# Optimization experiments

Measured on AMD Instinct MI355X. Metric: run time of the kernel, lower is better.

The kernel has to match this reference:

```python
import jax, jax.numpy as jnp
import numpy as np

BS, N_LINKS, MAX_LEN = 8192, 512, 32
D_LINK, D_PATH, D_READ, N_OUT = 32, 128, 256, 3
BN_EPS = 1e-5


def setup_inputs() -> dict:
    key = jax.random.key(0)
    ks = jax.random.split(key, 16)
    capa = jax.random.uniform(ks[0], (BS, N_LINKS), jnp.float32, 0.5, 1.0) * 100.0
    avail = jax.random.uniform(ks[1], (BS, N_LINKS), jnp.float32) * capa
    loss = jax.random.uniform(ks[2], (BS, N_LINKS), jnp.float32) * 0.05
    demand = jax.random.uniform(ks[3], (BS,), jnp.float32) * 10.0
    path = jax.random.randint(ks[4], (BS, MAX_LEN), 0, N_LINKS)
    hop_num = jax.random.randint(ks[5], (BS,), 1, MAX_LEN + 1)
    s = 0.1
    inp = {
        "demand": demand,
        "link_avail_capacity": avail,
        "link_capacity": capa,
        "link_loss": loss,
        "path": path,
        "hop_num": hop_num,
        # GRU params (PyTorch layout: [3H, D] gates ordered r,z,n)
        "gru_w_ih": jax.random.normal(ks[6], (3 * D_PATH, D_LINK), jnp.float32) * s,
        "gru_w_hh": jax.random.normal(ks[7], (3 * D_PATH, D_PATH), jnp.float32) * s,
        "gru_b_ih": jax.random.normal(ks[8], (3 * D_PATH,), jnp.float32) * s,
        "gru_b_hh": jax.random.normal(ks[9], (3 * D_PATH,), jnp.float32) * s,
        "bn_gamma": jnp.ones((D_PATH,), jnp.float32),
        "bn_beta": jnp.zeros((D_PATH,), jnp.float32),
        # stacked readout heads [N_OUT, ...]
        "rW1": jax.random.normal(ks[10], (N_OUT, D_PATH, D_READ), jnp.float32) * s,
        "rb1": jnp.zeros((N_OUT, D_READ), jnp.float32),
        "rW2": jax.random.normal(ks[11], (N_OUT, D_READ, D_READ), jnp.float32) * s,
        "rb2": jnp.zeros((N_OUT, D_READ), jnp.float32),
        "rW3": jax.random.normal(ks[12], (N_OUT, D_READ, 1), jnp.float32) * s,
        "rb3": jnp.zeros((N_OUT, 1), jnp.float32),
    }
    return inp


def _gru_scan(x_bt, h0, w_ih, w_hh, b_ih, b_hh):
    # x_bt: [B, T, D]; h0: [B, H] -> outputs [B, T, H]
    H = h0.shape[-1]
    def step(h, x_t):
        gi = x_t @ w_ih.T + b_ih          # [B, 3H]
        gh = h @ w_hh.T + b_hh            # [B, 3H]
        i_r, i_z, i_n = gi[:, :H], gi[:, H:2*H], gi[:, 2*H:]
        h_r, h_z, h_n = gh[:, :H], gh[:, H:2*H], gh[:, 2*H:]
        r = jax.nn.sigmoid(i_r + h_r)
        z = jax.nn.sigmoid(i_z + h_z)
        n = jnp.tanh(i_n + r * h_n)
        h_new = (1.0 - z) * n + z * h
        return h_new, h_new
    _, outs = jax.lax.scan(step, h0, jnp.swapaxes(x_bt, 0, 1))
    return jnp.swapaxes(outs, 0, 1)


def reference(demand, link_avail_capacity, link_capacity, link_loss, path, hop_num,
              gru_w_ih, gru_w_hh, gru_b_ih, gru_b_hh, bn_gamma, bn_beta,
              rW1, rb1, rW2, rb2, rW3, rb3):
    bs, n_links = link_capacity.shape
    max_len = path.shape[1]
    max_capa = jax.lax.stop_gradient(jnp.max(link_capacity))
    # link_state: [B, n_links, D_LINK]; first D_LINK-4 channels are zeros
    feats = jnp.stack([
        link_avail_capacity / max_capa,
        link_capacity / max_capa,
        link_avail_capacity / link_capacity,
        link_loss,
    ], axis=-1)
    link_state = jnp.concatenate(
        [jnp.zeros((bs, n_links, D_LINK - 4), feats.dtype), feats], axis=-1)
    link_state = jax.lax.stop_gradient(link_state)  # original detaches
    # initial hidden: zeros except last channel = demand/max_capa
    h0 = jnp.concatenate(
        [jnp.zeros((bs, D_PATH - 1), feats.dtype), (demand / max_capa)[:, None]], axis=-1)
    # fused gather of link states along each path, masked past hop_num
    gathered = jnp.take_along_axis(link_state, path[:, :, None], axis=1)  # [B, T, D]
    mask = (jnp.arange(max_len)[None, :] < hop_num[:, None])[:, :, None]
    link_inputs = gathered * mask.astype(gathered.dtype)
    outputs = _gru_scan(link_inputs, h0, gru_w_ih, gru_w_hh, gru_b_ih, gru_b_hh)
    # extract hidden state at last hop of each path
    idx = (hop_num - 1)[:, None, None]
    flow = jnp.take_along_axis(outputs, idx, axis=1)[:, 0, :]  # [B, H]
    # BatchNorm1d (training mode: batch statistics, biased variance)
    mean = jnp.mean(flow, axis=0)
    var = jnp.mean((flow - mean) ** 2, axis=0)
    flow = (flow - mean) * jax.lax.rsqrt(var + BN_EPS) * bn_gamma + bn_beta
    # readout heads: Linear -> SELU -> Linear -> SELU -> Linear
    h1 = jax.nn.selu(jnp.einsum('bh,uhr->ubr', flow, rW1) + rb1[:, None, :])
    h2 = jax.nn.selu(jnp.einsum('ubr,urs->ubs', h1, rW2) + rb2[:, None, :])
    y = jnp.einsum('ubs,uso->ubo', h2, rW3) + rb3[:, None, :]  # [U, B, 1]
    return jnp.transpose(y[:, :, 0], (1, 0))  # [B, U]
```

## Files before the change

### kernel.cpp

```cpp
#include <hip/hip_runtime.h>


#define BS 8192
#define NL 512
#define ML 32
#define DP 128
#define DR 256
#define NJOB 512
#define ST 172

#define OFF_SUM    64
#define OFF_SSQ    192
#define OFF_CUR    576
#define OFF_PERM   640
#define OFF_WHH16  (OFF_PERM + BS)
#define OFF_W1     (OFF_WHH16 + 24576)
#define OFF_W2     (OFF_W1 + 49152)
#define OFF_FEATS  (OFF_W2 + 98304)
#define OFF_FLOW   (OFF_FEATS + BS*ML*4)

#define FEATS_BLOCKS 1024
#define MAX_BLOCKS   256
#define WPREP_BLOCKS 1344
#define SORT_BID     (FEATS_BLOCKS + MAX_BLOCKS + WPREP_BLOCKS)
#define PREP_GRID    (SORT_BID + 1)

typedef _Float16 f16x8 __attribute__((ext_vector_type(8)));
typedef float    f32x4 __attribute__((ext_vector_type(4)));

__device__ __forceinline__ float sigmoidf_(float x){ return 1.0f/(1.0f+__expf(-x)); }
__device__ __forceinline__ float tanhf_(float x){
  float t = __expf(-2.0f*fabsf(x));
  float r = (1.0f-t)/(1.0f+t);
  return copysignf(r, x);
}
__device__ __forceinline__ float seluf_(float x){
  const float sc = 1.0507009873554805f, al = 1.6732632423543772f;
  return x > 0.0f ? sc*x : sc*al*(__expf(x)-1.0f);
}

__global__ void prep_all(const int* __restrict__ path, const int* __restrict__ hop,
                         const float* __restrict__ avail, const float* __restrict__ capa,
                         const float* __restrict__ loss, const float* __restrict__ whh,
                         const float* __restrict__ rW1, const float* __restrict__ rW2,
                         float* ws){
  const int bid = blockIdx.x;
  const int tid = threadIdx.x;

  if (bid < FEATS_BLOCKS){
    int idx = bid*256 + tid;
    int b = idx >> 5, t = idx & 31;
    float4 f = make_float4(0.f, 0.f, 0.f, 0.f);
    if (t < hop[b]){
      int l = path[idx];
      float a = avail[b*NL + l];
      float c = capa [b*NL + l];
      f.x = a; f.y = c; f.z = a / c; f.w = loss[b*NL + l];
    }
    ((float4*)(ws + OFF_FEATS))[idx] = f;
  } else if (bid < FEATS_BLOCKS + MAX_BLOCKS){
    const float4* c4 = (const float4*)capa;
    const int n4 = BS*NL/4;
    float m = 0.0f;
    for (int i = (bid - FEATS_BLOCKS)*256 + tid; i < n4; i += MAX_BLOCKS*256){
      float4 v = c4[i];
      m = fmaxf(m, fmaxf(fmaxf(v.x, v.y), fmaxf(v.z, v.w)));
    }
    #pragma unroll
    for (int o = 32; o > 0; o >>= 1) m = fmaxf(m, __shfl_down(m, o, 64));
    if ((tid & 63) == 0) atomicMax((int*)ws, __float_as_int(m));
  } else if (bid < SORT_BID){
    _Float16* whh16 = (_Float16*)(ws + OFF_WHH16);
    _Float16* w1    = (_Float16*)(ws + OFF_W1);
    _Float16* w2    = (_Float16*)(ws + OFF_W2);
    int i = (bid - FEATS_BLOCKS - MAX_BLOCKS)*256 + tid;
    if (i < 49152){
      whh16[i] = (_Float16)whh[i];
    } else if (i < 147456){
      int j = i - 49152; int u = j >> 15; int rem = j & 32767; int n = rem >> 7; int k = rem & 127;
      w1[j] = (_Float16)rW1[u*32768 + k*256 + n];
    } else if (i < 344064){
      int j = i - 147456; int u = j >> 16; int rem = j & 65535; int n = rem >> 8; int k = rem & 255;
      w2[j] = (_Float16)rW2[u*65536 + k*256 + n];
    }
  } else {
    __shared__ int hist[32], start[32];
    for (int i = 64 + tid; i < 640; i += 256) ws[i] = 0.0f;
    if (tid < 32) hist[tid] = 0;
    __syncthreads();
    for (int b = tid; b < BS; b += 256) atomicAdd(&hist[32 - hop[b]], 1);
    __syncthreads();
    if (tid == 0){ int acc = 0; for (int i = 0; i < 32; ++i){ start[i] = acc; acc += hist[i]; } }
    __syncthreads();
    int* perm = (int*)ws + OFF_PERM;
    for (int b = tid; b < BS; b += 256){
      int pos = atomicAdd(&start[32 - hop[b]], 1);
      perm[pos] = b;
    }
  }
}

__launch_bounds__(512, 4)
__global__ void kgru(const float* __restrict__ demand, const int* __restrict__ hop,
                     const float* __restrict__ wih, const float* __restrict__ bih,
                     const float* __restrict__ bhh, float* __restrict__ ws,
                     float* __restrict__ flow){
  __shared__ _Float16 hHI[2][16*ST];
  __shared__ _Float16 hLO[2][16*ST];
  const int tid  = threadIdx.x;
  const int w    = tid >> 6;
  const int lane = tid & 63;
  const int lm   = lane & 15;
  const int qd   = lane >> 4;
  const int ch   = w*16 + lm;
  const float inv_maxc = 1.0f / ws[0];
  const int* perm = (const int*)ws + OFF_PERM;
  const float* feats = ws + OFF_FEATS;
  const _Float16* whh16 = (const _Float16*)(ws + OFF_WHH16);

  const int bid = blockIdx.x;
  const int q = (bid < 256) ? bid : 767 - bid;

  for (int idx = tid; idx < 1024; idx += 512){
    const int buf = idx >> 9;
    const int rem = idx & 511;
    const int m   = rem >> 5;
    const int c   = 128 + (rem & 31);
    hHI[buf][m*ST + c] = (_Float16)0.f;
    hLO[buf][m*ST + c] = (_Float16)0.f;
  }

  f16x8 bfr[5], bfz[5], bfnh[4], bfni;
  #pragma unroll
  for (int kc = 0; kc < 4; ++kc){
    bfr[kc]  = *(const f16x8*)(whh16 + (      ch)*128 + kc*32 + qd*8);
    bfz[kc]  = *(const f16x8*)(whh16 + (128 + ch)*128 + kc*32 + qd*8);
    bfnh[kc] = *(const f16x8*)(whh16 + (256 + ch)*128 + kc*32 + qd*8);
  }
  bfr[4] = (f16x8)0; bfz[4] = (f16x8)0; bfni = (f16x8)0;
  if (qd == 0){
    #pragma unroll
    for (int j = 0; j < 4; ++j){
      float s = (j < 2) ? inv_maxc : 1.0f;
      bfr[4][j] = (_Float16)(wih[(      ch)*32 + 28 + j] * s);
      bfz[4][j] = (_Float16)(wih[(128 + ch)*32 + 28 + j] * s);
      bfni[j]   = (_Float16)(wih[(256 + ch)*32 + 28 + j] * s);
    }
  }
  const float bR  = bih[ch]     + bhh[ch];
  const float bZ  = bih[128+ch] + bhh[128+ch];
  const float bNI = bih[256+ch];
  const float bNH = bhh[256+ch];

  int it[4], hp[4];
  #pragma unroll
  for (int r = 0; r < 4; ++r){
    it[r] = perm[q*16 + qd*4 + r];
    hp[r] = hop[it[r]];
  }
  int tmax = max(max(hp[0],hp[1]), max(hp[2],hp[3]));
  tmax = max(tmax, __shfl_xor(tmax, 16, 64));
  tmax = max(tmax, __shfl_xor(tmax, 32, 64));

  const int fw_i = w*2 + (lane >> 2);
  const int fw_c = lane & 3;
  const bool fw  = (lane < 8);
  const int  fw_b = fw ? perm[q*16 + fw_i] : 0;

  __syncthreads();

  float hprev[4];
  #pragma unroll
  for (int r = 0; r < 4; ++r){
    float h0 = (ch == 127) ? demand[it[r]] * inv_maxc : 0.0f;
    hprev[r] = h0;
    const int m = qd*4 + r;
    _Float16 hi = (_Float16)h0;
    hHI[0][m*ST + ch] = hi;
    hLO[0][m*ST + ch] = (_Float16)(h0 - (float)hi);
  }
  if (fw){
    float v = feats[(fw_b*ML + 0)*4 + fw_c];
    _Float16 hi = (_Float16)v;
    hHI[0][fw_i*ST + 128 + fw_c] = hi;
    hLO[0][fw_i*ST + 128 + fw_c] = (_Float16)(v - (float)hi);
  }
  __syncthreads();

  for (int t = 0; t < tmax; ++t){
    const int cur = t & 1, nxt = cur ^ 1;
    if (fw && (t+1) < ML){
      float v = feats[(fw_b*ML + t + 1)*4 + fw_c];
      _Float16 hi = (_Float16)v;
      hHI[nxt][fw_i*ST + 128 + fw_c] = hi;
      hLO[nxt][fw_i*ST + 128 + fw_c] = (_Float16)(v - (float)hi);
    }

    f32x4 accr = {0.f,0.f,0.f,0.f}, accz = {0.f,0.f,0.f,0.f};
    f32x4 accnh = {0.f,0.f,0.f,0.f}, accni = {0.f,0.f,0.f,0.f};
    #pragma unroll
    for (int kc = 0; kc < 5; ++kc){
      const int off = lm*ST + kc*32 + qd*8;
      f16x8 ahi = *(const f16x8*)(&hHI[cur][off]);
      f16x8 alo = *(const f16x8*)(&hLO[cur][off]);
      accr = __builtin_amdgcn_mfma_f32_16x16x32_f16(ahi, bfr[kc], accr, 0, 0, 0);
      accr = __builtin_amdgcn_mfma_f32_16x16x32_f16(alo, bfr[kc], accr, 0, 0, 0);
      accz = __builtin_amdgcn_mfma_f32_16x16x32_f16(ahi, bfz[kc], accz, 0, 0, 0);
      accz = __builtin_amdgcn_mfma_f32_16x16x32_f16(alo, bfz[kc], accz, 0, 0, 0);
      if (kc < 4){
        accnh = __builtin_amdgcn_mfma_f32_16x16x32_f16(ahi, bfnh[kc], accnh, 0, 0, 0);
        accnh = __builtin_amdgcn_mfma_f32_16x16x32_f16(alo, bfnh[kc], accnh, 0, 0, 0);
      } else {
        accni = __builtin_amdgcn_mfma_f32_16x16x32_f16(ahi, bfni, accni, 0, 0, 0);
        accni = __builtin_amdgcn_mfma_f32_16x16x32_f16(alo, bfni, accni, 0, 0, 0);
      }
    }

    #pragma unroll
    for (int r = 0; r < 4; ++r){
      float rr = sigmoidf_(accr[r] + bR);
      float zz = sigmoidf_(accz[r] + bZ);
      float nn = tanhf_(accni[r] + bNI + rr*(accnh[r] + bNH));
      float hn = fmaf(zz, hprev[r] - nn, nn);
      if (t < hp[r]) hprev[r] = hn;
      const int m = qd*4 + r;
      _Float16 hi = (_Float16)hprev[r];
      hHI[nxt][m*ST + ch] = hi;
      hLO[nxt][m*ST + ch] = (_Float16)(hprev[r] - (float)hi);
    }
    __syncthreads();
  }

  float ssum = 0.f, ssq = 0.f;
  #pragma unroll
  for (int r = 0; r < 4; ++r){
    float v = hprev[r];
    flow[it[r]*DP + ch] = v;
    ssum += v;
    ssq  = fmaf(v, v, ssq);
  }
  ssum += __shfl_xor(ssum, 16, 64);  ssum += __shfl_xor(ssum, 32, 64);
  ssq  += __shfl_xor(ssq,  16, 64);  ssq  += __shfl_xor(ssq,  32, 64);
  if (qd == 0){
    atomicAdd(&ws[OFF_SUM + ch], ssum);
    atomicAdd(&ws[OFF_SSQ + ch], ssq);
  }
}

__launch_bounds__(256, 3)
__global__ void kmlp(const float* __restrict__ flow, const float* __restrict__ ws,
                     const float* __restrict__ gamma, const float* __restrict__ beta,
                     const float* __restrict__ rb1, const float* __restrict__ rb2,
                     const float* __restrict__ rW3, const float* __restrict__ rb3,
                     float* __restrict__ out){
  __shared__ _Float16 x_lds[32*136];
  __shared__ _Float16 h1_lds[32*264];
  __shared__ float aa[DP], bb[DP];
  __shared__ float y_part[4][32];
  const int tid  = threadIdx.x;
  const int w    = tid >> 6;
  const int lane = tid & 63;
  const int lm   = lane & 15;
  const int qd   = lane >> 4;
  const int b0   = blockIdx.x * 32;
  const int u    = blockIdx.y;
  const _Float16* w1 = (const _Float16*)(ws + OFF_W1) + u*(DR*DP);
  const _Float16* w2 = (const _Float16*)(ws + OFF_W2) + u*(DR*DR);

  if (tid < DP){
    float m = ws[OFF_SUM + tid] * (1.0f/BS);
    float q = ws[OFF_SSQ + tid] * (1.0f/BS);
    float rstd = rsqrtf(q - m*m + 1e-5f);
    float a = rstd * gamma[tid];
    aa[tid] = a;
    bb[tid] = fmaf(-m, a, beta[tid]);
  }
  __syncthreads();

  for (int idx = tid; idx < 32*DP; idx += 256){
    int i = idx >> 7, h = idx & 127;
    x_lds[i*136 + h] = (_Float16)fmaf(flow[(b0 + i)*DP + h], aa[h], bb[h]);
  }
  __syncthreads();

  {
    f16x8 a1[2][4];
    #pragma unroll
    for (int mt = 0; mt < 2; ++mt)
      #pragma unroll
      for (int kc = 0; kc < 4; ++kc)
        a1[mt][kc] = *(const f16x8*)(&x_lds[(mt*16 + lm)*136 + kc*32 + qd*8]);
    for (int nt = 0; nt < 4; ++nt){
      const int n = (4*w + nt)*16 + lm;
      const float bias1 = rb1[u*DR + n];
      f16x8 b1[4];
      #pragma unroll
      for (int kc = 0; kc < 4; ++kc)
        b1[kc] = *(const f16x8*)(w1 + n*DP + kc*32 + qd*8);
      #pragma unroll
      for (int mt = 0; mt < 2; ++mt){
        f32x4 acc = {bias1, bias1, bias1, bias1};
        #pragma unroll
        for (int kc = 0; kc < 4; ++kc)
          acc = __builtin_amdgcn_mfma_f32_16x16x32_f16(a1[mt][kc], b1[kc], acc, 0, 0, 0);
        #pragma unroll
        for (int r = 0; r < 4; ++r)
          h1_lds[(mt*16 + qd*4 + r)*264 + n] = (_Float16)seluf_(acc[r]);
      }
    }
  }
  __syncthreads();

  {
    f16x8 a2[2][8];
    #pragma unroll
    for (int mt = 0; mt < 2; ++mt)
      #pragma unroll
      for (int kc = 0; kc < 8; ++kc)
        a2[mt][kc] = *(const f16x8*)(&h1_lds[(mt*16 + lm)*264 + kc*32 + qd*8]);
    float p[2][4] = {{0.f,0.f,0.f,0.f},{0.f,0.f,0.f,0.f}};
    for (int nt = 0; nt < 4; ++nt){
      const int n = (4*w + nt)*16 + lm;
      const float bias2 = rb2[u*DR + n];
      const float w3l   = rW3[u*DR + n];
      f16x8 b2[8];
      #pragma unroll
      for (int kc = 0; kc < 8; ++kc)
        b2[kc] = *(const f16x8*)(w2 + n*DR + kc*32 + qd*8);
      #pragma unroll
      for (int mt = 0; mt < 2; ++mt){
        f32x4 acc = {bias2, bias2, bias2, bias2};
        #pragma unroll
        for (int kc = 0; kc < 8; ++kc)
          acc = __builtin_amdgcn_mfma_f32_16x16x32_f16(a2[mt][kc], b2[kc], acc, 0, 0, 0);
        #pragma unroll
        for (int r = 0; r < 4; ++r)
          p[mt][r] += seluf_(acc[r]) * w3l;
      }
    }
    #pragma unroll
    for (int mt = 0; mt < 2; ++mt){
      #pragma unroll
      for (int r = 0; r < 4; ++r){
        float v = p[mt][r];
        v += __shfl_xor(v, 1, 64);
        v += __shfl_xor(v, 2, 64);
        v += __shfl_xor(v, 4, 64);
        v += __shfl_xor(v, 8, 64);
        if (lm == 0) y_part[w][mt*16 + qd*4 + r] = v;
      }
    }
  }
  __syncthreads();
  if (tid < 32){
    float y = y_part[0][tid] + y_part[1][tid] + y_part[2][tid] + y_part[3][tid] + rb3[u];
    out[(b0 + tid)*3 + u] = y;
  }
}

extern "C" void kernel_launch(void* const* d_in, const int* in_sizes, int n_in,
                              void* d_out, int out_size, void* d_ws, size_t ws_size,
                              hipStream_t stream){
  const float* demand = (const float*)d_in[0];
  const float* avail  = (const float*)d_in[1];
  const float* capa   = (const float*)d_in[2];
  const float* loss   = (const float*)d_in[3];
  const int*   path   = (const int*)d_in[4];
  const int*   hop    = (const int*)d_in[5];
  const float* wih    = (const float*)d_in[6];
  const float* whh    = (const float*)d_in[7];
  const float* bih    = (const float*)d_in[8];
  const float* bhh    = (const float*)d_in[9];
  const float* gamma  = (const float*)d_in[10];
  const float* beta   = (const float*)d_in[11];
  const float* rW1    = (const float*)d_in[12];
  const float* rb1    = (const float*)d_in[13];
  const float* rW2    = (const float*)d_in[14];
  const float* rb2    = (const float*)d_in[15];
  const float* rW3    = (const float*)d_in[16];
  const float* rb3    = (const float*)d_in[17];
  float* ws  = (float*)d_ws;
  float* out = (float*)d_out;

  prep_all <<<PREP_GRID, 256, 0, stream>>>(path, hop, avail, capa, loss,
                                           whh, rW1, rW2, ws);
  kgru     <<<NJOB, 512, 0, stream>>>(demand, hop, wih, bih, bhh, ws, ws + OFF_FLOW);
  kmlp     <<<dim3(BS/32, 3), 256, 0, stream>>>(ws + OFF_FLOW, ws, gamma, beta,
                                                rb1, rb2, rW3, rb3, out);
}
```

Baseline: 222.8 us.

## Fuse link-feature gather and Whh conversion into GRU kernel

Removes the separate prep stage that gathered per-hop link features into a workspace buffer and converted W_hh to fp16. The GRU kernel now gathers avail/capa/loss directly per step, prefetching one step ahead in a register, and converts W_hh from fp32 on load. This cuts a large workspace write and read and shrinks the prep grid, at the cost of dependent global loads (path then link data) inside the recurrent loop. Those loads may add latency to each step if the one-step prefetch does not hide them.

Result: slower. 242.1 us (+8.7%).

```diff
diff --git a/kernel.cpp b/kernel.cpp
--- a/kernel.cpp
+++ b/kernel.cpp
@@ -13,16 +13,13 @@
 #define OFF_SSQ    192
 #define OFF_CUR    576
 #define OFF_PERM   640
-#define OFF_WHH16  (OFF_PERM + BS)
-#define OFF_W1     (OFF_WHH16 + 24576)
+#define OFF_W1     (OFF_PERM + BS)
 #define OFF_W2     (OFF_W1 + 49152)
-#define OFF_FEATS  (OFF_W2 + 98304)
-#define OFF_FLOW   (OFF_FEATS + BS*ML*4)
-
-#define FEATS_BLOCKS 1024
+#define OFF_FLOW   (OFF_W2 + 98304)
+
 #define MAX_BLOCKS   256
-#define WPREP_BLOCKS 1344
-#define SORT_BID     (FEATS_BLOCKS + MAX_BLOCKS + WPREP_BLOCKS)
+#define WPREP_BLOCKS 1152
+#define SORT_BID     (MAX_BLOCKS + WPREP_BLOCKS)
 #define PREP_GRID    (SORT_BID + 1)
 
 typedef _Float16 f16x8 __attribute__((ext_vector_type(8)));
@@ -39,30 +36,17 @@
   return x > 0.0f ? sc*x : sc*al*(__expf(x)-1.0f);
 }
 
-__global__ void prep_all(const int* __restrict__ path, const int* __restrict__ hop,
-                         const float* __restrict__ avail, const float* __restrict__ capa,
-                         const float* __restrict__ loss, const float* __restrict__ whh,
-                         const float* __restrict__ rW1, const float* __restrict__ rW2,
-                         float* ws){
+__global__ void prep0(const int* __restrict__ hop, const float* __restrict__ capa,
+                      const float* __restrict__ rW1, const float* __restrict__ rW2,
+                      float* ws){
   const int bid = blockIdx.x;
   const int tid = threadIdx.x;
 
-  if (bid < FEATS_BLOCKS){
-    int idx = bid*256 + tid;
-    int b = idx >> 5, t = idx & 31;
-    float4 f = make_float4(0.f, 0.f, 0.f, 0.f);
-    if (t < hop[b]){
-      int l = path[idx];
-      float a = avail[b*NL + l];
-      float c = capa [b*NL + l];
-      f.x = a; f.y = c; f.z = a / c; f.w = loss[b*NL + l];
-    }
-    ((float4*)(ws + OFF_FEATS))[idx] = f;
-  } else if (bid < FEATS_BLOCKS + MAX_BLOCKS){
+  if (bid < MAX_BLOCKS){
     const float4* c4 = (const float4*)capa;
     const int n4 = BS*NL/4;
     float m = 0.0f;
-    for (int i = (bid - FEATS_BLOCKS)*256 + tid; i < n4; i += MAX_BLOCKS*256){
+    for (int i = bid*256 + tid; i < n4; i += MAX_BLOCKS*256){
       float4 v = c4[i];
       m = fmaxf(m, fmaxf(fmaxf(v.x, v.y), fmaxf(v.z, v.w)));
     }
@@ -70,17 +54,14 @@
     for (int o = 32; o > 0; o >>= 1) m = fmaxf(m, __shfl_down(m, o, 64));
     if ((tid & 63) == 0) atomicMax((int*)ws, __float_as_int(m));
   } else if (bid < SORT_BID){
-    _Float16* whh16 = (_Float16*)(ws + OFF_WHH16);
-    _Float16* w1    = (_Float16*)(ws + OFF_W1);
-    _Float16* w2    = (_Float16*)(ws + OFF_W2);
-    int i = (bid - FEATS_BLOCKS - MAX_BLOCKS)*256 + tid;
-    if (i < 49152){
-      whh16[i] = (_Float16)whh[i];
-    } else if (i < 147456){
-      int j = i - 49152; int u = j >> 15; int rem = j & 32767; int n = rem >> 7; int k = rem & 127;
+    _Float16* w1 = (_Float16*)(ws + OFF_W1);
+    _Float16* w2 = (_Float16*)(ws + OFF_W2);
+    int i = (bid - MAX_BLOCKS)*256 + tid;
+    if (i < 98304){
+      int j = i; int u = j >> 15; int rem = j & 32767; int n = rem >> 7; int k = rem & 127;
       w1[j] = (_Float16)rW1[u*32768 + k*256 + n];
-    } else if (i < 344064){
-      int j = i - 147456; int u = j >> 16; int rem = j & 65535; int n = rem >> 8; int k = rem & 255;
+    } else {
+      int j = i - 98304; int u = j >> 16; int rem = j & 65535; int n = rem >> 8; int k = rem & 255;
       w2[j] = (_Float16)rW2[u*65536 + k*256 + n];
     }
   } else {
@@ -102,9 +83,11 @@
 
 __launch_bounds__(512, 4)
 __global__ void kgru(const float* __restrict__ demand, const int* __restrict__ hop,
-                     const float* __restrict__ wih, const float* __restrict__ bih,
-                     const float* __restrict__ bhh, float* __restrict__ ws,
-                     float* __restrict__ flow){
+                     const int* __restrict__ path, const float* __restrict__ avail,
+                     const float* __restrict__ capa, const float* __restrict__ loss,
+                     const float* __restrict__ whh, const float* __restrict__ wih,
+                     const float* __restrict__ bih, const float* __restrict__ bhh,
+                     float* __restrict__ ws, float* __restrict__ flow){
   __shared__ _Float16 hHI[2][16*ST];
   __shared__ _Float16 hLO[2][16*ST];
   const int tid  = threadIdx.x;
@@ -115,8 +98,6 @@
   const int ch   = w*16 + lm;
   const float inv_maxc = 1.0f / ws[0];
   const int* perm = (const int*)ws + OFF_PERM;
-  const float* feats = ws + OFF_FEATS;
-  const _Float16* whh16 = (const _Float16*)(ws + OFF_WHH16);
 
   const int bid = blockIdx.x;
   const int q = (bid < 256) ? bid : 767 - bid;
@@ -133,9 +114,16 @@
   f16x8 bfr[5], bfz[5], bfnh[4], bfni;
   #pragma unroll
   for (int kc = 0; kc < 4; ++kc){
-    bfr[kc]  = *(const f16x8*)(whh16 + (      ch)*128 + kc*32 + qd*8);
-    bfz[kc]  = *(const f16x8*)(whh16 + (128 + ch)*128 + kc*32 + qd*8);
-    bfnh[kc] = *(const f16x8*)(whh16 + (256 + ch)*128 + kc*32 + qd*8);
+    const int ko = kc*32 + qd*8;
+    const float* pr = whh + (      ch)*128 + ko;
+    const float* pz = whh + (128 + ch)*128 + ko;
+    const float* pn = whh + (256 + ch)*128 + ko;
+    #pragma unroll
+    for (int j = 0; j < 8; ++j){
+      bfr[kc][j]  = (_Float16)pr[j];
+      bfz[kc][j]  = (_Float16)pz[j];
+      bfnh[kc][j] = (_Float16)pn[j];
+    }
   }
   bfr[4] = (f16x8)0; bfz[4] = (f16x8)0; bfni = (f16x8)0;
   if (qd == 0){
@@ -162,10 +150,11 @@
   tmax = max(tmax, __shfl_xor(tmax, 16, 64));
   tmax = max(tmax, __shfl_xor(tmax, 32, 64));
 
-  const int fw_i = w*2 + (lane >> 2);
-  const int fw_c = lane & 3;
-  const bool fw  = (lane < 8);
+  const int  fw_i = w*2 + (lane >> 2);
+  const int  fw_c = lane & 3;
+  const bool fw   = (lane < 8);
   const int  fw_b = fw ? perm[q*16 + fw_i] : 0;
+  float v_hold = 0.0f;
 
   __syncthreads();
 
@@ -180,20 +169,34 @@
     hLO[0][m*ST + ch] = (_Float16)(h0 - (float)hi);
   }
   if (fw){
-    float v = feats[(fw_b*ML + 0)*4 + fw_c];
-    _Float16 hi = (_Float16)v;
+    int l0 = path[fw_b*ML + 0];
+    int o0 = fw_b*NL + l0;
+    float v0 = (fw_c == 0) ? avail[o0] :
+               (fw_c == 1) ? capa [o0] :
+               (fw_c == 2) ? avail[o0] / capa[o0] : loss[o0];
+    _Float16 hi = (_Float16)v0;
     hHI[0][fw_i*ST + 128 + fw_c] = hi;
-    hLO[0][fw_i*ST + 128 + fw_c] = (_Float16)(v - (float)hi);
+    hLO[0][fw_i*ST + 128 + fw_c] = (_Float16)(v0 - (float)hi);
+    int l1 = path[fw_b*ML + 1];
+    int o1 = fw_b*NL + l1;
+    v_hold = (fw_c == 0) ? avail[o1] :
+             (fw_c == 1) ? capa [o1] :
+             (fw_c == 2) ? avail[o1] / capa[o1] : loss[o1];
   }
   __syncthreads();
 
   for (int t = 0; t < tmax; ++t){
     const int cur = t & 1, nxt = cur ^ 1;
-    if (fw && (t+1) < ML){
-      float v = feats[(fw_b*ML + t + 1)*4 + fw_c];
-      _Float16 hi = (_Float16)v;
+    if (fw){
+      _Float16 hi = (_Float16)v_hold;
       hHI[nxt][fw_i*ST + 128 + fw_c] = hi;
-      hLO[nxt][fw_i*ST + 128 + fw_c] = (_Float16)(v - (float)hi);
+      hLO[nxt][fw_i*ST + 128 + fw_c] = (_Float16)(v_hold - (float)hi);
+      int tt = (t + 2 < ML) ? t + 2 : ML - 1;
+      int l  = path[fw_b*ML + tt];
+      int o  = fw_b*NL + l;
+      v_hold = (fw_c == 0) ? avail[o] :
+               (fw_c == 1) ? capa [o] :
+               (fw_c == 2) ? avail[o] / capa[o] : loss[o];
     }
 
     f32x4 accr = {0.f,0.f,0.f,0.f}, accz = {0.f,0.f,0.f,0.f};
@@ -382,9 +385,9 @@
   float* ws  = (float*)d_ws;
   float* out = (float*)d_out;
 
-  prep_all <<<PREP_GRID, 256, 0, stream>>>(path, hop, avail, capa, loss,
-                                           whh, rW1, rW2, ws);
-  kgru     <<<NJOB, 512, 0, stream>>>(demand, hop, wih, bih, bhh, ws, ws + OFF_FLOW);
-  kmlp     <<<dim3(BS/32, 3), 256, 0, stream>>>(ws + OFF_FLOW, ws, gamma, beta,
-                                                rb1, rb2, rW3, rb3, out);
-}
+  prep0 <<<PREP_GRID, 256, 0, stream>>>(hop, capa, rW1, rW2, ws);
+  kgru  <<<NJOB, 512, 0, stream>>>(demand, hop, path, avail, capa, loss,
+                                   whh, wih, bih, bhh, ws, ws + OFF_FLOW);
+  kmlp  <<<dim3(BS/32, 3), 256, 0, stream>>>(ws + OFF_FLOW, ws, gamma, beta,
+                                             rb1, rb2, rW3, rb3, out);
+}
```
